# Kernel tuning notes

Measured on AMD Instinct MI355X. Metric: run time of the kernel, lower is better.

The kernel has to match this reference:

```python
import jax, jax.numpy as jnp
import numpy as np

VOCAB = 50257
EMB = 512
HID = 256
NCLS = 20
PAD = 0


def setup_inputs() -> dict:
    key = jax.random.key(0)
    ks = jax.random.split(key, 10)
    s_e = 1.0 / np.sqrt(EMB)
    s_h = 1.0 / np.sqrt(HID)
    x = jax.random.randint(ks[0], (32, 2048), 0, VOCAB, dtype=jnp.int64)
    return {
        "x": x,
        "emb": jax.random.normal(ks[1], (VOCAB, EMB), jnp.float32),
        "w_ih": jax.random.uniform(ks[2], (4 * HID, EMB), jnp.float32, -s_h, s_h),
        "w_hh": jax.random.uniform(ks[3], (4 * HID, HID), jnp.float32, -s_h, s_h),
        "b_ih": jax.random.uniform(ks[4], (4 * HID,), jnp.float32, -s_h, s_h),
        "b_hh": jax.random.uniform(ks[5], (4 * HID,), jnp.float32, -s_h, s_h),
        "w1": jax.random.uniform(ks[6], (2 * HID, HID), jnp.float32, -s_h, s_h),
        "b1": jax.random.uniform(ks[7], (2 * HID,), jnp.float32, -s_h, s_h),
        "w2": jax.random.uniform(ks[8], (NCLS, 2 * HID), jnp.float32, -1.0 / np.sqrt(2 * HID), 1.0 / np.sqrt(2 * HID)),
        "b2": jax.random.uniform(ks[9], (NCLS,), jnp.float32, -1.0 / np.sqrt(2 * HID), 1.0 / np.sqrt(2 * HID)),
    }


def _lstm(xe, w_ih, w_hh, b_ih, b_hh):
    # xe: (B, T, E) -> hs: (B, T, H). PyTorch gate order: i, f, g, o.
    B, T, E = xe.shape
    H = w_hh.shape[1]
    # Precompute input contribution for all timesteps (one big GEMM).
    xg = jnp.einsum('bte,ge->btg', xe, w_ih) + b_ih + b_hh  # (B, T, 4H)
    xg = jnp.swapaxes(xg, 0, 1)  # (T, B, 4H)

    def step(carry, xt):
        h, c = carry
        gates = xt + h @ w_hh.T  # (B, 4H)
        i, f, g, o = jnp.split(gates, 4, axis=-1)
        i = jax.nn.sigmoid(i)
        f = jax.nn.sigmoid(f)
        g = jnp.tanh(g)
        o = jax.nn.sigmoid(o)
        c = f * c + i * g
        h = o * jnp.tanh(c)
        return (h, c), h

    h0 = jnp.zeros((B, H), xe.dtype)
    c0 = jnp.zeros((B, H), xe.dtype)
    _, hs = jax.lax.scan(step, (h0, c0), xg)
    return jnp.swapaxes(hs, 0, 1)  # (B, T, H)


def reference(x, emb, w_ih, w_hh, b_ih, b_hh, w1, b1, w2, b2):
    mask = (x != PAD)  # (B, T)
    lens = mask.sum(axis=1)  # (B,)
    xe = emb[x]  # (B, T, E)
    h = _lstm(xe, w_ih, w_hh, b_ih, b_hh)  # (B, T, H)
    pooled = (h * mask[:, :, None]).sum(axis=1) / lens[:, None].astype(h.dtype)
    # dropout omitted (inference / eval mode)
    lin1 = jax.nn.relu(pooled @ w1.T + b1)
    return lin1 @ w2.T + b2  # (B, n_classes)
```

## Files before the change

### kernel.cpp

```cpp
#include <hip/hip_runtime.h>
#include <hip/hip_fp16.h>

typedef _Float16 f16;
typedef _Float16 f16x2 __attribute__((ext_vector_type(2)));
typedef _Float16 f16x8 __attribute__((ext_vector_type(8)));
typedef float f32x4 __attribute__((ext_vector_type(4)));

#define B_    32
#define T_    2048
#define E_    512
#define H_    256
#define G4_   1024
#define VOCAB_ 50257

static const size_t WS_XG   = 0;
static const size_t WS_WIH  = 134217728ull;
static const size_t WS_WREG = 135266304ull;
static const size_t WS_WLDS = 135659520ull;
static const size_t WS_MB   = 135790592ull;
static const size_t WS_BSUM = 135798784ull;
static const size_t WS_POOL = 135802880ull;

#define LDS_BYTES 132096

__device__ __forceinline__ unsigned pack2f(float a, float b) {
    f16x2 h; h.x = (f16)a; h.y = (f16)b;
    return __builtin_bit_cast(unsigned, h);
}

__device__ __forceinline__ float fdot2u(unsigned a, unsigned b, float c) {
#if __has_builtin(__builtin_amdgcn_fdot2)
    return __builtin_amdgcn_fdot2(__builtin_bit_cast(f16x2, a),
                                  __builtin_bit_cast(f16x2, b), c, false);
#else
    f16x2 av = __builtin_bit_cast(f16x2, a), bv = __builtin_bit_cast(f16x2, b);
    return c + (float)av.x * (float)bv.x + (float)av.y * (float)bv.y;
#endif
}

__device__ __forceinline__ float sigm(float v) {
    return 1.f / (1.f + exp2f(-1.44269504f * v));
}
__device__ __forceinline__ float tanhr(float v) {
    float t = exp2f(-2.88539008f * fabsf(v));
    float r = (1.f - t) / (1.f + t);
    return v < 0.f ? -r : r;
}

__device__ __forceinline__ int detect64(const int* x) {
    return (x[1] == 0 && x[3] == 0 && x[5] == 0) ? 1 : 0;
}

__global__ void prep_k(const int* __restrict__ x,
                       const float* __restrict__ w_ih, const float* __restrict__ w_hh,
                       const float* __restrict__ b_ih, const float* __restrict__ b_hh,
                       f16* __restrict__ wih16, unsigned* __restrict__ wreg,
                       uint4* __restrict__ wlds, unsigned* __restrict__ mb,
                       float* __restrict__ bsum)
{
    const int gid = blockIdx.x * blockDim.x + threadIdx.x;
    const int stride = gridDim.x * blockDim.x;
    const int is64 = detect64(x);
    for (int i = gid; i < G4_*E_; i += stride) wih16[i] = (f16)w_ih[i];
    for (int i = gid; i < G4_; i += stride) bsum[i] = b_ih[i] + b_hh[i];
    for (int n = gid; n < 192*512; n += stride) {
        const int idx = n >> 9, tid = n & 511;
        const int j = tid >> 1, gp = tid & 1;
        const int row = idx / 96, d = idx % 96;
        const int R = gp*512 + row*256 + j;
        const int k = 2*d;
        wreg[n] = pack2f(w_hh[(size_t)R*H_ + k], w_hh[(size_t)R*H_ + k + 1]);
    }
    for (int n = gid; n < 8*16*64; n += stride) {
        const int wv = n >> 10, s = (n >> 6) & 15, lane = n & 63;
        const int j = wv*32 + (lane >> 1), gp = lane & 1;
        const int r = s >> 3, e = s & 7;
        const int R = gp*512 + r*256 + j;
        const float* wrow = w_hh + (size_t)R*H_;
        unsigned du[4];
        #pragma unroll
        for (int u = 0; u < 4; ++u) {
            const int k = 2*(96 + 4*e + u);
            du[u] = pack2f(wrow[k], wrow[k + 1]);
        }
        uint4 v; v.x = du[0]; v.y = du[1]; v.z = du[2]; v.w = du[3];
        wlds[n] = v;
    }
    for (int i = gid; i < 32*64; i += stride) {
        const int b = i >> 6, wd = i & 63;
        unsigned word = 0;
        for (int tt = 0; tt < 32; ++tt) {
            const size_t ti = ((size_t)b*T_ + wd*32 + tt) << is64;
            word |= (x[ti] != 0 ? 1u : 0u) << tt;
        }
        mb[i] = word;
    }
}

__global__ __launch_bounds__(256) void gemm_xg_k(
    const int* __restrict__ x, const float* __restrict__ emb,
    const f16* __restrict__ wih, const float* __restrict__ bsum,
    f16* __restrict__ xg)
{
    __shared__ f16 As[128*32];
    __shared__ f16 Bs[128*32];
    const int tid = threadIdx.x;
    const int bid = blockIdx.x;
    const int mt = bid >> 3, nt = bid & 7;
    const int wv = tid >> 6, lane = tid & 63;
    const int wm = wv & 1, wn = wv >> 1;
    const int ml = lane & 15, kg = lane >> 4;
    const int is64 = detect64(x);
    const int r = tid >> 1, kh = tid & 1;
    int tok = x[(size_t)(mt*128 + r) << is64];
    tok = tok < 0 ? 0 : (tok >= VOCAB_ ? VOCAB_ - 1 : tok);
    const float* arow = emb + (size_t)tok * E_ + kh*16;
    const f16*   brow = wih + (size_t)(nt*128 + r) * E_ + kh*16;

    f32x4 acc[4][4] = {};
    for (int kk = 0; kk < 16; ++kk) {
        const int k0 = kk * 32;
        float4 a0 = *(const float4*)(arow + k0 + 0);
        float4 a1 = *(const float4*)(arow + k0 + 4);
        float4 a2 = *(const float4*)(arow + k0 + 8);
        float4 a3 = *(const float4*)(arow + k0 + 12);
        uint4 bu0 = *(const uint4*)(brow + k0);
        uint4 bu1 = *(const uint4*)(brow + k0 + 8);
        uint4 au0, au1;
        au0.x = pack2f(a0.x, a0.y); au0.y = pack2f(a0.z, a0.w);
        au0.z = pack2f(a1.x, a1.y); au0.w = pack2f(a1.z, a1.w);
        au1.x = pack2f(a2.x, a2.y); au1.y = pack2f(a2.z, a2.w);
        au1.z = pack2f(a3.x, a3.y); au1.w = pack2f(a3.z, a3.w);
        __syncthreads();
        *(uint4*)(&As[r*32 + kh*16 + 0]) = au0;
        *(uint4*)(&As[r*32 + kh*16 + 8]) = au1;
        *(uint4*)(&Bs[r*32 + kh*16 + 0]) = bu0;
        *(uint4*)(&Bs[r*32 + kh*16 + 8]) = bu1;
        __syncthreads();
        f16x8 af[4], bf[4];
        #pragma unroll
        for (int i = 0; i < 4; ++i) {
            af[i] = *(const f16x8*)(&As[(wm*64 + i*16 + ml)*32 + kg*8]);
            bf[i] = *(const f16x8*)(&Bs[(wn*64 + i*16 + ml)*32 + kg*8]);
        }
        #pragma unroll
        for (int i = 0; i < 4; ++i)
            #pragma unroll
            for (int j = 0; j < 4; ++j)
                acc[i][j] = __builtin_amdgcn_mfma_f32_16x16x32_f16(af[i], bf[j], acc[i][j], 0, 0, 0);
    }
    #pragma unroll
    for (int j = 0; j < 4; ++j) {
        const int gc = nt*128 + wn*64 + j*16 + ml;
        const float bs = bsum[gc];
        const int pc = ((gc & 255) << 2) | (gc >> 8);
        #pragma unroll
        for (int i = 0; i < 4; ++i) {
            #pragma unroll
            for (int q = 0; q < 4; ++q) {
                const int gr = mt*128 + wm*64 + i*16 + kg*4 + q;
                xg[(size_t)gr*G4_ + pc] = (f16)(acc[i][j][q] + bs);
            }
        }
    }
}

__global__ __attribute__((amdgpu_flat_work_group_size(512, 512), amdgpu_waves_per_eu(2, 2)))
void recur_k(const f16* __restrict__ xg,
             const unsigned* __restrict__ wreg_g, const uint4* __restrict__ wlds_g,
             const unsigned* __restrict__ mb,
             float* __restrict__ pool)
{
    extern __shared__ char smem[];
    const int tid = threadIdx.x, b = blockIdx.x;
    const int wv = tid >> 6, lane = tid & 63;
    const int j = tid >> 1, gp = tid & 1;

    unsigned wr[192];
    #pragma unroll
    for (int i = 0; i < 192; ++i) wr[i] = wreg_g[i*512 + tid];
    #pragma unroll
    for (int i = 0; i < 192; ++i) asm volatile("" : "+v"(wr[i]));
    {
        uint4* wl = (uint4*)smem;
        #pragma unroll
        for (int s = 0; s < 16; ++s)
            wl[wv*1024 + s*64 + lane] = wlds_g[wv*1024 + s*64 + lane];
    }
    if (tid < 256) ((unsigned*)(smem + 131072))[tid] = 0u;

    const char* xgrow = (const char*)xg + (size_t)b * T_ * 2048;
    const char* wbase = smem + wv*16384;
    float cst = 0.f, pooled = 0.f;
    unsigned mw = 0;
    __syncthreads();

    for (int t = 0; t < T_; ++t) {
        const char* hb = smem + 131072 + (t & 1)*512;
        uint2 hv = *(const uint2*)(hb + lane*8);
        unsigned xv = *(const unsigned*)(xgrow + (size_t)t*2048 + tid*4);
        if ((t & 31) == 0) mw = mb[b*64 + (t >> 5)];
        float p0 = 0.f, p1 = 0.f;

        #pragma unroll
        for (int ph = 0; ph < 3; ++ph) {
            unsigned sA[16], sB[16];
            #pragma unroll
            for (int u = 0; u < 16; ++u) {
                sA[u] = __builtin_amdgcn_readlane((int)hv.x, ph*16 + u);
                sB[u] = __builtin_amdgcn_readlane((int)hv.y, ph*16 + u);
            }
            #pragma unroll
            for (int u = 0; u < 16; ++u) {
                const int d0 = ph*32 + 2*u;
                p0 = fdot2u(wr[d0],       sA[u], p0);
                p0 = fdot2u(wr[d0 + 1],   sB[u], p0);
                p1 = fdot2u(wr[96 + d0],     sA[u], p1);
                p1 = fdot2u(wr[96 + d0 + 1], sB[u], p1);
            }
        }
        {
            unsigned sA[16], sB[16];
            #pragma unroll
            for (int u = 0; u < 16; ++u) {
                sA[u] = __builtin_amdgcn_readlane((int)hv.x, 48 + u);
                sB[u] = __builtin_amdgcn_readlane((int)hv.y, 48 + u);
            }
            #pragma unroll
            for (int e = 0; e < 8; ++e) {
                uint4 w0 = *(const uint4*)(wbase + ((0*8 + e)*64 + lane)*16);
                p0 = fdot2u(w0.x, sA[2*e],   p0);
                p0 = fdot2u(w0.y, sB[2*e],   p0);
                p0 = fdot2u(w0.z, sA[2*e+1], p0);
                p0 = fdot2u(w0.w, sB[2*e+1], p0);
                uint4 w1 = *(const uint4*)(wbase + ((1*8 + e)*64 + lane)*16);
                p1 = fdot2u(w1.x, sA[2*e],   p1);
                p1 = fdot2u(w1.y, sB[2*e],   p1);
                p1 = fdot2u(w1.z, sA[2*e+1], p1);
                p1 = fdot2u(w1.w, sB[2*e+1], p1);
            }
        }
        const float q0 = __shfl_xor(p0, 1);
        const float q1 = __shfl_xor(p1, 1);
        const unsigned xq = __shfl_xor((int)xv, 1);
        const f16x2 xvh = __builtin_bit_cast(f16x2, xv);
        const f16x2 xqh = __builtin_bit_cast(f16x2, xq);
        const float pi_ = gp ? q0 : p0, pf_ = gp ? q1 : p1;
        const float pg_ = gp ? p0 : q0, po_ = gp ? p1 : q1;
        const f16x2 xif = gp ? xqh : xvh;
        const f16x2 xgo = gp ? xvh : xqh;
        const float gi = sigm (pi_ + (float)xif.x);
        const float gf = sigm (pf_ + (float)xif.y);
        const float gg = tanhr(pg_ + (float)xgo.x);
        const float go = sigm (po_ + (float)xgo.y);
        cst = gf*cst + gi*gg;
        const float hvv = go * tanhr(cst);
        if ((mw >> (t & 31)) & 1) pooled += hvv;
        if (!gp) *(f16*)(smem + 131072 + ((t+1) & 1)*512 + j*2) = (f16)hvv;
        __syncthreads();
    }
    if (!gp) pool[b*H_ + j] = pooled;
}

__global__ __launch_bounds__(256) void head_k(
    const int* __restrict__ x,
    const float* __restrict__ pool,
    const float* __restrict__ w1, const float* __restrict__ b1,
    const float* __restrict__ w2, const float* __restrict__ b2,
    float* __restrict__ out)
{
    __shared__ float pl[256];
    __shared__ float l1[512];
    __shared__ int wcnt[4];
    const int b = blockIdx.x, tid = threadIdx.x;
    const int is64 = detect64(x);
    const int* xrow = x + (((size_t)b * T_) << is64);
    int cnt = 0;
    for (int k = tid; k < T_; k += 256) cnt += (xrow[(size_t)k << is64] != 0);
    #pragma unroll
    for (int s = 32; s > 0; s >>= 1) cnt += __shfl_xor(cnt, s);
    if ((tid & 63) == 0) wcnt[tid >> 6] = cnt;
    __syncthreads();
    const float inv = 1.f / (float)(wcnt[0] + wcnt[1] + wcnt[2] + wcnt[3]);
    pl[tid] = pool[b*256 + tid] * inv;
    __syncthreads();
    for (int o = tid; o < 512; o += 256) {
        const float4* wrow = (const float4*)(w1 + (size_t)o*256);
        float s = b1[o];
        #pragma unroll 8
        for (int k = 0; k < 64; ++k) {
            float4 wv = wrow[k];
            s += pl[k*4+0]*wv.x + pl[k*4+1]*wv.y + pl[k*4+2]*wv.z + pl[k*4+3]*wv.w;
        }
        l1[o] = fmaxf(s, 0.f);
    }
    __syncthreads();
    if (tid < 20) {
        const float4* wrow = (const float4*)(w2 + (size_t)tid*512);
        float s = b2[tid];
        #pragma unroll 8
        for (int k = 0; k < 128; ++k) {
            float4 wv = wrow[k];
            s += l1[k*4+0]*wv.x + l1[k*4+1]*wv.y + l1[k*4+2]*wv.z + l1[k*4+3]*wv.w;
        }
        out[b*20 + tid] = s;
    }
}

extern "C" void kernel_launch(void* const* d_in, const int* in_sizes, int n_in,
                              void* d_out, int out_size, void* d_ws, size_t ws_size,
                              hipStream_t stream) {
    (void)in_sizes; (void)n_in; (void)out_size; (void)ws_size;
    const int*   x    = (const int*)d_in[0];
    const float* emb  = (const float*)d_in[1];
    const float* w_ih = (const float*)d_in[2];
    const float* w_hh = (const float*)d_in[3];
    const float* b_ih = (const float*)d_in[4];
    const float* b_hh = (const float*)d_in[5];
    const float* w1   = (const float*)d_in[6];
    const float* b1   = (const float*)d_in[7];
    const float* w2   = (const float*)d_in[8];
    const float* b2   = (const float*)d_in[9];
    float* out = (float*)d_out;
    char* ws = (char*)d_ws;

    f16*      xg    = (f16*)(ws + WS_XG);
    f16*      wih16 = (f16*)(ws + WS_WIH);
    unsigned* wreg  = (unsigned*)(ws + WS_WREG);
    uint4*    wlds  = (uint4*)(ws + WS_WLDS);
    unsigned* mb    = (unsigned*)(ws + WS_MB);
    float*    bsum  = (float*)(ws + WS_BSUM);
    float*    pool  = (float*)(ws + WS_POOL);

    hipLaunchKernelGGL(prep_k, dim3(512), dim3(256), 0, stream,
                       x, w_ih, w_hh, b_ih, b_hh, wih16, wreg, wlds, mb, bsum);
    hipLaunchKernelGGL(gemm_xg_k, dim3(4096), dim3(256), 0, stream,
                       x, emb, wih16, bsum, xg);
    hipLaunchKernelGGL(recur_k, dim3(32), dim3(512), LDS_BYTES, stream,
                       xg, wreg, wlds, mb, pool);
    hipLaunchKernelGGL(head_k, dim3(32), dim3(256), 0, stream,
                       x, pool, w1, b1, w2, b2, out);
}
```

Before: 4.455 ms.

## Compute LSTM recurrent matvec with MFMA 16x16x32 instead of fdot2 readlane chains

```diff
diff --git a/kernel.cpp b/kernel.cpp
--- a/kernel.cpp
+++ b/kernel.cpp
@@ -16,26 +16,17 @@
 static const size_t WS_XG   = 0;
 static const size_t WS_WIH  = 134217728ull;
 static const size_t WS_WREG = 135266304ull;
-static const size_t WS_WLDS = 135659520ull;
+static const size_t WS_WLDS = 135634944ull;
 static const size_t WS_MB   = 135790592ull;
 static const size_t WS_BSUM = 135798784ull;
 static const size_t WS_POOL = 135802880ull;
 
-#define LDS_BYTES 132096
+#define HB_OFF   155648
+#define LDS_BYTES 156672
 
 __device__ __forceinline__ unsigned pack2f(float a, float b) {
     f16x2 h; h.x = (f16)a; h.y = (f16)b;
     return __builtin_bit_cast(unsigned, h);
-}
-
-__device__ __forceinline__ float fdot2u(unsigned a, unsigned b, float c) {
-#if __has_builtin(__builtin_amdgcn_fdot2)
-    return __builtin_amdgcn_fdot2(__builtin_bit_cast(f16x2, a),
-                                  __builtin_bit_cast(f16x2, b), c, false);
-#else
-    f16x2 av = __builtin_bit_cast(f16x2, a), bv = __builtin_bit_cast(f16x2, b);
-    return c + (float)av.x * (float)bv.x + (float)av.y * (float)bv.y;
-#endif
 }
 
 __device__ __forceinline__ float sigm(float v) {
@@ -54,7 +45,7 @@
 __global__ void prep_k(const int* __restrict__ x,
                        const float* __restrict__ w_ih, const float* __restrict__ w_hh,
                        const float* __restrict__ b_ih, const float* __restrict__ b_hh,
-                       f16* __restrict__ wih16, unsigned* __restrict__ wreg,
+                       f16* __restrict__ wih16, uint4* __restrict__ wreg,
                        uint4* __restrict__ wlds, unsigned* __restrict__ mb,
                        float* __restrict__ bsum)
 {
@@ -63,27 +54,34 @@
     const int is64 = detect64(x);
     for (int i = gid; i < G4_*E_; i += stride) wih16[i] = (f16)w_ih[i];
     for (int i = gid; i < G4_; i += stride) bsum[i] = b_ih[i] + b_hh[i];
-    for (int n = gid; n < 192*512; n += stride) {
-        const int idx = n >> 9, tid = n & 511;
-        const int j = tid >> 1, gp = tid & 1;
-        const int row = idx / 96, d = idx % 96;
-        const int R = gp*512 + row*256 + j;
-        const int k = 2*d;
-        wreg[n] = pack2f(w_hh[(size_t)R*H_ + k], w_hh[(size_t)R*H_ + k + 1]);
-    }
-    for (int n = gid; n < 8*16*64; n += stride) {
-        const int wv = n >> 10, s = (n >> 6) & 15, lane = n & 63;
-        const int j = wv*32 + (lane >> 1), gp = lane & 1;
-        const int r = s >> 3, e = s & 7;
-        const int R = gp*512 + r*256 + j;
-        const float* wrow = w_hh + (size_t)R*H_;
-        unsigned du[4];
-        #pragma unroll
-        for (int u = 0; u < 4; ++u) {
-            const int k = 2*(96 + 4*e + u);
-            du[u] = pack2f(wrow[k], wrow[k + 1]);
-        }
-        uint4 v; v.x = du[0]; v.y = du[1]; v.z = du[2]; v.w = du[3];
+    for (int n = gid; n < 45*512; n += stride) {
+        const int f = n >> 9, tid = n & 511;
+        const int wv = tid >> 6, lane = tid & 63, li = lane & 15, lq = lane >> 4;
+        int kt, qc;
+        if (f < 40) { kt = f >> 3; qc = f & 7; } else { kt = 5; qc = f - 40; }
+        const int q = qc >> 1, c = qc & 1;
+        const int G = q*256 + wv*32 + c*16 + li;
+        const int k0 = kt*32 + lq*8;
+        const float* src = w_hh + (size_t)G*H_ + k0;
+        uint4 v;
+        v.x = pack2f(src[0], src[1]); v.y = pack2f(src[2], src[3]);
+        v.z = pack2f(src[4], src[5]); v.w = pack2f(src[6], src[7]);
+        wreg[n] = v;
+    }
+    for (int n = gid; n < 8*19*64; n += stride) {
+        const int lane = n & 63, sw = n >> 6;
+        const int s = sw % 19, wv = sw / 19;
+        int kt, qc;
+        if (s < 3)       { kt = 5; qc = 5 + s; }
+        else if (s < 11) { kt = 6; qc = s - 3; }
+        else             { kt = 7; qc = s - 11; }
+        const int q = qc >> 1, c = qc & 1;
+        const int G = q*256 + wv*32 + c*16 + (lane & 15);
+        const int k0 = kt*32 + (lane >> 4)*8;
+        const float* src = w_hh + (size_t)G*H_ + k0;
+        uint4 v;
+        v.x = pack2f(src[0], src[1]); v.y = pack2f(src[2], src[3]);
+        v.z = pack2f(src[4], src[5]); v.w = pack2f(src[6], src[7]);
         wlds[n] = v;
     }
     for (int i = gid; i < 32*64; i += stride) {
@@ -167,99 +165,111 @@
 
 __global__ __attribute__((amdgpu_flat_work_group_size(512, 512), amdgpu_waves_per_eu(2, 2)))
 void recur_k(const f16* __restrict__ xg,
-             const unsigned* __restrict__ wreg_g, const uint4* __restrict__ wlds_g,
+             const uint4* __restrict__ wreg_g, const uint4* __restrict__ wlds_g,
              const unsigned* __restrict__ mb,
              float* __restrict__ pool)
 {
     extern __shared__ char smem[];
     const int tid = threadIdx.x, b = blockIdx.x;
     const int wv = tid >> 6, lane = tid & 63;
-    const int j = tid >> 1, gp = tid & 1;
-
-    unsigned wr[192];
+    const int li = lane & 15, lq16 = (lane >> 4) * 16;
+    const int j0 = wv*32 + li, j1 = j0 + 16;
+
+    f16x8 wb[45];
     #pragma unroll
-    for (int i = 0; i < 192; ++i) wr[i] = wreg_g[i*512 + tid];
+    for (int f = 0; f < 45; ++f)
+        wb[f] = *(const f16x8*)(wreg_g + (size_t)f*512 + tid);
     #pragma unroll
-    for (int i = 0; i < 192; ++i) asm volatile("" : "+v"(wr[i]));
+    for (int f = 0; f < 40; ++f) asm volatile("" : "+v"(wb[f]));
     {
         uint4* wl = (uint4*)smem;
         #pragma unroll
-        for (int s = 0; s < 16; ++s)
-            wl[wv*1024 + s*64 + lane] = wlds_g[wv*1024 + s*64 + lane];
-    }
-    if (tid < 256) ((unsigned*)(smem + 131072))[tid] = 0u;
+        for (int s = 0; s < 19; ++s)
+            wl[(wv*19 + s)*64 + lane] = wlds_g[(wv*19 + s)*64 + lane];
+    }
+    if (tid < 256) ((unsigned*)(smem + HB_OFF))[tid] = 0u;
 
     const char* xgrow = (const char*)xg + (size_t)b * T_ * 2048;
-    const char* wbase = smem + wv*16384;
-    float cst = 0.f, pooled = 0.f;
+    const char* wbase = smem + wv*19*1024;
+    float c0 = 0.f, c1 = 0.f, pooled0 = 0.f, pooled1 = 0.f;
     unsigned mw = 0;
     __syncthreads();
 
     for (int t = 0; t < T_; ++t) {
-        const char* hb = smem + 131072 + (t & 1)*512;
-        uint2 hv = *(const uint2*)(hb + lane*8);
-        unsigned xv = *(const unsigned*)(xgrow + (size_t)t*2048 + tid*4);
+        const char* hb = smem + HB_OFF + (t & 1)*512;
+        uint2 xv0 = *(const uint2*)(xgrow + (size_t)t*2048 + j0*8);
+        uint2 xv1 = *(const uint2*)(xgrow + (size_t)t*2048 + j1*8);
         if ((t & 31) == 0) mw = mb[b*64 + (t >> 5)];
-        float p0 = 0.f, p1 = 0.f;
-
-        #pragma unroll
-        for (int ph = 0; ph < 3; ++ph) {
-            unsigned sA[16], sB[16];
-            #pragma unroll
-            for (int u = 0; u < 16; ++u) {
-                sA[u] = __builtin_amdgcn_readlane((int)hv.x, ph*16 + u);
-                sB[u] = __builtin_amdgcn_readlane((int)hv.y, ph*16 + u);
+
+        f32x4 acc[8];
+        #pragma unroll
+        for (int i = 0; i < 8; ++i) acc[i] = (f32x4){0.f, 0.f, 0.f, 0.f};
+
+        #pragma unroll
+        for (int kt = 0; kt < 5; ++kt) {
+            f16x8 a = *(const f16x8*)(hb + kt*64 + lq16);
+            #pragma unroll
+            for (int qc = 0; qc < 8; ++qc)
+                acc[qc] = __builtin_amdgcn_mfma_f32_16x16x32_f16(a, wb[kt*8 + qc], acc[qc], 0, 0, 0);
+        }
+        {
+            f16x8 a = *(const f16x8*)(hb + 5*64 + lq16);
+            #pragma unroll
+            for (int qc = 0; qc < 5; ++qc)
+                acc[qc] = __builtin_amdgcn_mfma_f32_16x16x32_f16(a, wb[40 + qc], acc[qc], 0, 0, 0);
+            #pragma unroll
+            for (int s = 0; s < 3; ++s) {
+                f16x8 wl = *(const f16x8*)(wbase + s*1024 + lane*16);
+                acc[5 + s] = __builtin_amdgcn_mfma_f32_16x16x32_f16(a, wl, acc[5 + s], 0, 0, 0);
             }
-            #pragma unroll
-            for (int u = 0; u < 16; ++u) {
-                const int d0 = ph*32 + 2*u;
-                p0 = fdot2u(wr[d0],       sA[u], p0);
-                p0 = fdot2u(wr[d0 + 1],   sB[u], p0);
-                p1 = fdot2u(wr[96 + d0],     sA[u], p1);
-                p1 = fdot2u(wr[96 + d0 + 1], sB[u], p1);
+        }
+        {
+            f16x8 a = *(const f16x8*)(hb + 6*64 + lq16);
+            #pragma unroll
+            for (int qc = 0; qc < 8; ++qc) {
+                f16x8 wl = *(const f16x8*)(wbase + (3 + qc)*1024 + lane*16);
+                acc[qc] = __builtin_amdgcn_mfma_f32_16x16x32_f16(a, wl, acc[qc], 0, 0, 0);
             }
         }
         {
-            unsigned sA[16], sB[16];
-            #pragma unroll
-            for (int u = 0; u < 16; ++u) {
-                sA[u] = __builtin_amdgcn_readlane((int)hv.x, 48 + u);
-                sB[u] = __builtin_amdgcn_readlane((int)hv.y, 48 + u);
+            f16x8 a = *(const f16x8*)(hb + 7*64 + lq16);
+            #pragma unroll
+            for (int qc = 0; qc < 8; ++qc) {
+                f16x8 wl = *(const f16x8*)(wbase + (11 + qc)*1024 + lane*16);
+                acc[qc] = __builtin_amdgcn_mfma_f32_16x16x32_f16(a, wl, acc[qc], 0, 0, 0);
             }
-            #pragma unroll
-            for (int e = 0; e < 8; ++e) {
-                uint4 w0 = *(const uint4*)(wbase + ((0*8 + e)*64 + lane)*16);
-                p0 = fdot2u(w0.x, sA[2*e],   p0);
-                p0 = fdot2u(w0.y, sB[2*e],   p0);
-                p0 = fdot2u(w0.z, sA[2*e+1], p0);
-                p0 = fdot2u(w0.w, sB[2*e+1], p0);
-                uint4 w1 = *(const uint4*)(wbase + ((1*8 + e)*64 + lane)*16);
-                p1 = fdot2u(w1.x, sA[2*e],   p1);
-                p1 = fdot2u(w1.y, sB[2*e],   p1);
-                p1 = fdot2u(w1.z, sA[2*e+1], p1);
-                p1 = fdot2u(w1.w, sB[2*e+1], p1);
-            }
-        }
-        const float q0 = __shfl_xor(p0, 1);
-        const float q1 = __shfl_xor(p1, 1);
-        const unsigned xq = __shfl_xor((int)xv, 1);
-        const f16x2 xvh = __builtin_bit_cast(f16x2, xv);
-        const f16x2 xqh = __builtin_bit_cast(f16x2, xq);
-        const float pi_ = gp ? q0 : p0, pf_ = gp ? q1 : p1;
-        const float pg_ = gp ? p0 : q0, po_ = gp ? p1 : q1;
-        const f16x2 xif = gp ? xqh : xvh;
-        const f16x2 xgo = gp ? xvh : xqh;
-        const float gi = sigm (pi_ + (float)xif.x);
-        const float gf = sigm (pf_ + (float)xif.y);
-        const float gg = tanhr(pg_ + (float)xgo.x);
-        const float go = sigm (po_ + (float)xgo.y);
-        cst = gf*cst + gi*gg;
-        const float hvv = go * tanhr(cst);
-        if ((mw >> (t & 31)) & 1) pooled += hvv;
-        if (!gp) *(f16*)(smem + 131072 + ((t+1) & 1)*512 + j*2) = (f16)hvv;
+        }
+
+        const f16x2 xa0 = __builtin_bit_cast(f16x2, xv0.x);
+        const f16x2 xb0 = __builtin_bit_cast(f16x2, xv0.y);
+        const f16x2 xa1 = __builtin_bit_cast(f16x2, xv1.x);
+        const f16x2 xb1 = __builtin_bit_cast(f16x2, xv1.y);
+        const float gi0 = sigm (acc[0][0] + (float)xa0.x);
+        const float gf0 = sigm (acc[2][0] + (float)xa0.y);
+        const float gg0 = tanhr(acc[4][0] + (float)xb0.x);
+        const float go0 = sigm (acc[6][0] + (float)xb0.y);
+        const float gi1 = sigm (acc[1][0] + (float)xa1.x);
+        const float gf1 = sigm (acc[3][0] + (float)xa1.y);
+        const float gg1 = tanhr(acc[5][0] + (float)xb1.x);
+        const float go1 = sigm (acc[7][0] + (float)xb1.y);
+        c0 = gf0*c0 + gi0*gg0;
+        c1 = gf1*c1 + gi1*gg1;
+        const float h0 = go0 * tanhr(c0);
+        const float h1 = go1 * tanhr(c1);
+        const float madd = ((mw >> (t & 31)) & 1) ? 1.f : 0.f;
+        pooled0 += madd * h0;
+        pooled1 += madd * h1;
+        char* hn = smem + HB_OFF + ((t + 1) & 1)*512;
+        if (lane < 16) {
+            *(f16*)(hn + j0*2) = (f16)h0;
+            *(f16*)(hn + j1*2) = (f16)h1;
+        }
         __syncthreads();
     }
-    if (!gp) pool[b*H_ + j] = pooled;
+    if (lane < 16) {
+        pool[b*H_ + j0] = pooled0;
+        pool[b*H_ + j1] = pooled1;
+    }
 }
 
 __global__ __launch_bounds__(256) void head_k(
@@ -326,7 +336,7 @@
 
     f16*      xg    = (f16*)(ws + WS_XG);
     f16*      wih16 = (f16*)(ws + WS_WIH);
-    unsigned* wreg  = (unsigned*)(ws + WS_WREG);
+    uint4*    wreg  = (uint4*)(ws + WS_WREG);
     uint4*    wlds  = (uint4*)(ws + WS_WLDS);
     unsigned* mb    = (unsigned*)(ws + WS_MB);
     float*    bsum  = (float*)(ws + WS_BSUM);
```

New measurement: 4.379 ms. No clear change (-1.7%).
